# Performance work log

Measured on AMD Instinct MI355X. Metric: run time of the kernel, lower is better.

## Reference

```python
import jax, jax.numpy as jnp
import numpy as np

D_IN = 1024
D_OUT = 1024
N = 4096


def setup_inputs() -> dict:
    key = jax.random.key(0)
    kx, kq, kk, kv = jax.random.split(key, 4)
    s = 1.0 / np.sqrt(D_IN)
    return {
        "x": jax.random.normal(kx, (N, D_IN), dtype=jnp.float32),
        # nn.Linear weights stored as [d_out, d_in]
        "wq": jax.random.uniform(kq, (D_OUT, D_IN), dtype=jnp.float32, minval=-s, maxval=s),
        "wk": jax.random.uniform(kk, (D_OUT, D_IN), dtype=jnp.float32, minval=-s, maxval=s),
        "wv": jax.random.uniform(kv, (D_OUT, D_IN), dtype=jnp.float32, minval=-s, maxval=s),
    }


def reference(x, wq, wk, wv):
    q = x @ wq.T  # [N, d_out]
    k = x @ wk.T
    v = x @ wv.T
    scores = q @ k.T  # [N, N]
    weights = jax.nn.softmax(scores / jnp.sqrt(jnp.asarray(k.shape[-1], x.dtype)), axis=-1)
    return weights @ v  # [N, d_out]
```

## Files before the change

### kernel.cpp

```cpp
#include <hip/hip_runtime.h>
#include <cstdint>

#define NTOK 4096
#define DMODEL 1024

typedef __bf16 bf16x8 __attribute__((ext_vector_type(8)));
typedef float f32x4 __attribute__((ext_vector_type(4)));

__device__ __forceinline__ unsigned short f32_to_bf16(float f) {
    unsigned int u = __float_as_uint(f);
    unsigned int r = 0x7FFFu + ((u >> 16) & 1u);
    return (unsigned short)((u + r) >> 16);
}

__global__ __launch_bounds__(256) void cvt_f32_bf16(const float* __restrict__ in,
                                                    unsigned short* __restrict__ out,
                                                    int n4) {
    int i = blockIdx.x * 256 + threadIdx.x;
    if (i >= n4) return;
    float4 v = reinterpret_cast<const float4*>(in)[i];
    ushort4 o;
    o.x = f32_to_bf16(v.x);
    o.y = f32_to_bf16(v.y);
    o.z = f32_to_bf16(v.z);
    o.w = f32_to_bf16(v.w);
    reinterpret_cast<ushort4*>(out)[i] = o;
}

#define BM 128
#define BN 128
#define BK 64

#define STAGE_TILES(Ablk, lda, Bblk, ldb, k0)                                        \
    _Pragma("unroll") for (int i = 0; i < 4; ++i) {                                  \
        const int c = tid + i * 256;                                                 \
        const int row = c >> 3;                                                      \
        const int jl = (c & 7) ^ (row & 7);                                          \
        const unsigned short* ga = (Ablk) + (size_t)row * (lda) + ((k0) + jl * 8);   \
        const unsigned short* gb = (Bblk) + (size_t)row * (ldb) + ((k0) + jl * 8);   \
        __builtin_amdgcn_global_load_lds(                                            \
            (const __attribute__((address_space(1))) void*)ga,                       \
            (__attribute__((address_space(3))) void*)(&As[c * 8]), 16, 0, 0);        \
        __builtin_amdgcn_global_load_lds(                                            \
            (const __attribute__((address_space(1))) void*)gb,                       \
            (__attribute__((address_space(3))) void*)(&Bs[c * 8]), 16, 0, 0);        \
    }

#define COMPUTE_TILE()                                                               \
    _Pragma("unroll") for (int ks = 0; ks < 2; ++ks) {                               \
        bf16x8 af[4], bfr[4];                                                        \
        _Pragma("unroll") for (int m = 0; m < 4; ++m) {                              \
            const int row = wr * 64 + m * 16 + (lane & 15);                          \
            const int ch = (ks * 4 + (lane >> 4)) ^ (row & 7);                       \
            af[m] = *reinterpret_cast<const bf16x8*>(                                \
                reinterpret_cast<const char*>(As) + row * 128 + ch * 16);            \
        }                                                                            \
        _Pragma("unroll") for (int n = 0; n < 4; ++n) {                              \
            const int row = wc * 64 + n * 16 + (lane & 15);                          \
            const int ch = (ks * 4 + (lane >> 4)) ^ (row & 7);                       \
            bfr[n] = *reinterpret_cast<const bf16x8*>(                               \
                reinterpret_cast<const char*>(Bs) + row * 128 + ch * 16);            \
        }                                                                            \
        _Pragma("unroll") for (int m = 0; m < 4; ++m)                                \
            _Pragma("unroll") for (int n = 0; n < 4; ++n)                            \
                acc[m][n] = __builtin_amdgcn_mfma_f32_16x16x32_bf16(                 \
                    af[m], bfr[n], acc[m][n], 0, 0, 0);                              \
    }

__global__ __launch_bounds__(256, 2) void gemm_scores(
    const unsigned short* __restrict__ QK, float* __restrict__ S) {
    __shared__ __align__(16) unsigned short As[BM * BK];
    __shared__ __align__(16) unsigned short Bs[BN * BK];
    const int tid = threadIdx.x;
    const int lane = tid & 63;
    const int wave = tid >> 6;
    const int wr = wave >> 1, wc = wave & 1;

    const int id = blockIdx.x;
    const int g = id & 7, s = id >> 3;
    const int bx = s >> 2;
    const int by = (g << 2) + (s & 3);

    const unsigned short* Ablk = QK + (size_t)by * BM * 2048;
    const unsigned short* Bblk = QK + 1024 + (size_t)bx * BN * 2048;
    f32x4 acc[4][4] = {};

    for (int k0 = 0; k0 < DMODEL; k0 += BK) {
        STAGE_TILES(Ablk, 2048, Bblk, 2048, k0)
        __syncthreads();
        COMPUTE_TILE()
        __syncthreads();
    }

    const int col0 = bx * BN + wc * 64 + (lane & 15);
    const int row0 = by * BM + wr * 64 + ((lane >> 4) << 2);
#pragma unroll
    for (int m = 0; m < 4; ++m)
#pragma unroll
        for (int n = 0; n < 4; ++n)
#pragma unroll
            for (int r = 0; r < 4; ++r)
                S[(size_t)(row0 + m * 16 + r) * NTOK + (col0 + n * 16)] = acc[m][n][r];
}

__global__ __launch_bounds__(256, 2) void gemm_qkv(
    const unsigned short* __restrict__ xb, const unsigned short* __restrict__ Wb,
    unsigned short* __restrict__ QK, unsigned short* __restrict__ Vt) {
    __shared__ __align__(16) unsigned short As[BM * BK];
    __shared__ __align__(16) unsigned short Bs[BN * BK];
    const int tid = threadIdx.x;
    const int lane = tid & 63;
    const int wave = tid >> 6;
    const int wr = wave >> 1, wc = wave & 1;

    const int id = blockIdx.x;
    const int g = id & 7, s = id >> 3;
    const int bx = s % 24;
    const int by = (g << 2) + s / 24;

    const unsigned short* Ablk = xb + (size_t)by * BM * DMODEL;
    const unsigned short* Bblk = Wb + (size_t)bx * BN * DMODEL;
    f32x4 acc[4][4] = {};

    for (int k0 = 0; k0 < DMODEL; k0 += BK) {
        STAGE_TILES(Ablk, DMODEL, Bblk, DMODEL, k0)
        __syncthreads();
        COMPUTE_TILE()
        __syncthreads();
    }

    const int colw = wc * 64 + (lane & 15);
    const int row0 = by * BM + wr * 64 + ((lane >> 4) << 2);
    if (bx < 16) {
        const int col0 = bx * 128 + colw;
#pragma unroll
        for (int m = 0; m < 4; ++m)
#pragma unroll
            for (int n = 0; n < 4; ++n)
#pragma unroll
                for (int r = 0; r < 4; ++r)
                    QK[(size_t)(row0 + m * 16 + r) * 2048 + (col0 + n * 16)] =
                        f32_to_bf16(acc[m][n][r]);
    } else {
        const int vrow0 = (bx - 16) * 128 + colw;
#pragma unroll
        for (int m = 0; m < 4; ++m)
#pragma unroll
            for (int n = 0; n < 4; ++n) {
                ushort4 o;
                o.x = f32_to_bf16(acc[m][n][0]);
                o.y = f32_to_bf16(acc[m][n][1]);
                o.z = f32_to_bf16(acc[m][n][2]);
                o.w = f32_to_bf16(acc[m][n][3]);
                *reinterpret_cast<ushort4*>(
                    &Vt[(size_t)(vrow0 + n * 16) * NTOK + (row0 + m * 16)]) = o;
            }
    }
}

__global__ __launch_bounds__(256, 2) void gemm_pv(
    const unsigned short* __restrict__ P, const unsigned short* __restrict__ Vt,
    float* __restrict__ C) {
    __shared__ __align__(16) unsigned short As[BM * BK];
    __shared__ __align__(16) unsigned short Bs[BN * BK];
    const int tid = threadIdx.x;
    const int lane = tid & 63;
    const int wave = tid >> 6;
    const int wr = wave >> 1, wc = wave & 1;

    const int id = blockIdx.x;
    const int g = id & 7, s = id >> 3;
    const int bx = s & 7;
    const int by = (g << 2) + (s >> 3);

    const unsigned short* Ablk = P + (size_t)by * BM * (2 * NTOK);
    const unsigned short* Bblk = Vt + (size_t)bx * BN * NTOK;
    f32x4 acc[4][4] = {};

    for (int k0 = 0; k0 < NTOK; k0 += BK) {
        STAGE_TILES(Ablk, 2 * NTOK, Bblk, NTOK, k0)
        __syncthreads();
        COMPUTE_TILE()
        __syncthreads();
    }

    const int col0 = bx * BN + wc * 64 + (lane & 15);
    const int row0 = by * BM + wr * 64 + ((lane >> 4) << 2);
#pragma unroll
    for (int m = 0; m < 4; ++m)
#pragma unroll
        for (int n = 0; n < 4; ++n)
#pragma unroll
            for (int r = 0; r < 4; ++r)
                C[(size_t)(row0 + m * 16 + r) * DMODEL + (col0 + n * 16)] = acc[m][n][r];
}

__global__ __launch_bounds__(256) void softmax_rows(float* __restrict__ S, int N) {
    const int row = blockIdx.x;
    float* s = S + (size_t)row * N;
    const int t = threadIdx.x;

    float v[16];
    float mx = -1e30f;
#pragma unroll
    for (int i = 0; i < 4; ++i) {
        float4 x = reinterpret_cast<const float4*>(s)[t + i * 256];
        v[i * 4 + 0] = x.x;
        v[i * 4 + 1] = x.y;
        v[i * 4 + 2] = x.z;
        v[i * 4 + 3] = x.w;
        mx = fmaxf(mx, fmaxf(fmaxf(x.x, x.y), fmaxf(x.z, x.w)));
    }
#pragma unroll
    for (int off = 32; off; off >>= 1) mx = fmaxf(mx, __shfl_xor(mx, off));
    __shared__ float redm[4];
    if (!(t & 63)) redm[t >> 6] = mx;
    __syncthreads();
    mx = fmaxf(fmaxf(redm[0], redm[1]), fmaxf(redm[2], redm[3]));

    float sum = 0.f;
#pragma unroll
    for (int i = 0; i < 16; ++i) {
        v[i] = __expf((v[i] - mx) * 0.03125f);
        sum += v[i];
    }
#pragma unroll
    for (int off = 32; off; off >>= 1) sum += __shfl_xor(sum, off);
    __shared__ float reds[4];
    if (!(t & 63)) reds[t >> 6] = sum;
    __syncthreads();
    sum = (reds[0] + reds[1]) + (reds[2] + reds[3]);
    const float inv = 1.0f / sum;

    unsigned short* p = reinterpret_cast<unsigned short*>(s);
#pragma unroll
    for (int i = 0; i < 4; ++i) {
        ushort4 o;
        o.x = f32_to_bf16(v[i * 4 + 0] * inv);
        o.y = f32_to_bf16(v[i * 4 + 1] * inv);
        o.z = f32_to_bf16(v[i * 4 + 2] * inv);
        o.w = f32_to_bf16(v[i * 4 + 3] * inv);
        reinterpret_cast<ushort4*>(p)[t + i * 256] = o;
    }
}

extern "C" void kernel_launch(void* const* d_in, const int* in_sizes, int n_in,
                              void* d_out, int out_size, void* d_ws, size_t ws_size,
                              hipStream_t stream) {
    (void)in_sizes; (void)n_in; (void)out_size; (void)ws_size;
    const float* x = (const float*)d_in[0];
    const float* wq = (const float*)d_in[1];
    const float* wk = (const float*)d_in[2];
    const float* wv = (const float*)d_in[3];
    float* out = (float*)d_out;

    const size_t MB = 1ull << 20;
    char* w = (char*)d_ws;
    unsigned short* xb = (unsigned short*)(w + 0 * MB);
    unsigned short* Wb = (unsigned short*)(w + 8 * MB);
    unsigned short* QK = (unsigned short*)(w + 14 * MB);
    unsigned short* Vt = (unsigned short*)(w + 30 * MB);
    float* S           = (float*)(w + 38 * MB);

    cvt_f32_bf16<<<4096, 256, 0, stream>>>(x, xb, (NTOK * DMODEL) / 4);
    cvt_f32_bf16<<<1024, 256, 0, stream>>>(wq, Wb, (DMODEL * DMODEL) / 4);
    cvt_f32_bf16<<<1024, 256, 0, stream>>>(wk, Wb + DMODEL * DMODEL, (DMODEL * DMODEL) / 4);
    cvt_f32_bf16<<<1024, 256, 0, stream>>>(wv, Wb + 2 * DMODEL * DMODEL, (DMODEL * DMODEL) / 4);

    gemm_qkv<<<768, 256, 0, stream>>>(xb, Wb, QK, Vt);

    gemm_scores<<<1024, 256, 0, stream>>>(QK, S);

    softmax_rows<<<NTOK, 256, 0, stream>>>(S, NTOK);

    gemm_pv<<<256, 256, 0, stream>>>((const unsigned short*)S, Vt, out);
}
```

Baseline: 229.1 us.

## Double-buffer LDS tiles in all GEMMs and halve PV tile width for more blocks

Adds ping-pong LDS buffers to the QKV, scores and PV GEMMs so global-to-LDS loads for the next K tile are issued while MFMAs run on the current one, removing one barrier per step. The PV GEMM also shrinks its N tile from 128 to 64 and launches 512 blocks instead of 256, so the machine is filled better for that long-K GEMM. This doubles LDS use per block and can limit occupancy, and the smaller PV tile reloads P more often.

```diff
diff --git a/kernel.cpp b/kernel.cpp
--- a/kernel.cpp
+++ b/kernel.cpp
@@ -31,7 +31,7 @@
 #define BN 128
 #define BK 64
 
-#define STAGE_TILES(Ablk, lda, Bblk, ldb, k0)                                        \
+#define STAGE_DB(As_, Bs_, Ablk, lda, Bblk, ldb, k0)                                 \
     _Pragma("unroll") for (int i = 0; i < 4; ++i) {                                  \
         const int c = tid + i * 256;                                                 \
         const int row = c >> 3;                                                      \
@@ -40,26 +40,26 @@
         const unsigned short* gb = (Bblk) + (size_t)row * (ldb) + ((k0) + jl * 8);   \
         __builtin_amdgcn_global_load_lds(                                            \
             (const __attribute__((address_space(1))) void*)ga,                       \
-            (__attribute__((address_space(3))) void*)(&As[c * 8]), 16, 0, 0);        \
+            (__attribute__((address_space(3))) void*)(&(As_)[c * 8]), 16, 0, 0);     \
         __builtin_amdgcn_global_load_lds(                                            \
             (const __attribute__((address_space(1))) void*)gb,                       \
-            (__attribute__((address_space(3))) void*)(&Bs[c * 8]), 16, 0, 0);        \
-    }
-
-#define COMPUTE_TILE()                                                               \
+            (__attribute__((address_space(3))) void*)(&(Bs_)[c * 8]), 16, 0, 0);     \
+    }
+
+#define COMPUTE_DB(As_, Bs_)                                                         \
     _Pragma("unroll") for (int ks = 0; ks < 2; ++ks) {                               \
         bf16x8 af[4], bfr[4];                                                        \
         _Pragma("unroll") for (int m = 0; m < 4; ++m) {                              \
             const int row = wr * 64 + m * 16 + (lane & 15);                          \
             const int ch = (ks * 4 + (lane >> 4)) ^ (row & 7);                       \
             af[m] = *reinterpret_cast<const bf16x8*>(                                \
-                reinterpret_cast<const char*>(As) + row * 128 + ch * 16);            \
+                reinterpret_cast<const char*>(As_) + row * 128 + ch * 16);           \
         }                                                                            \
         _Pragma("unroll") for (int n = 0; n < 4; ++n) {                              \
             const int row = wc * 64 + n * 16 + (lane & 15);                          \
             const int ch = (ks * 4 + (lane >> 4)) ^ (row & 7);                       \
             bfr[n] = *reinterpret_cast<const bf16x8*>(                               \
-                reinterpret_cast<const char*>(Bs) + row * 128 + ch * 16);            \
+                reinterpret_cast<const char*>(Bs_) + row * 128 + ch * 16);           \
         }                                                                            \
         _Pragma("unroll") for (int m = 0; m < 4; ++m)                                \
             _Pragma("unroll") for (int n = 0; n < 4; ++n)                            \
@@ -69,8 +69,8 @@
 
 __global__ __launch_bounds__(256, 2) void gemm_scores(
     const unsigned short* __restrict__ QK, float* __restrict__ S) {
-    __shared__ __align__(16) unsigned short As[BM * BK];
-    __shared__ __align__(16) unsigned short Bs[BN * BK];
+    __shared__ __align__(16) unsigned short As0[BM * BK], Bs0[BN * BK];
+    __shared__ __align__(16) unsigned short As1[BM * BK], Bs1[BN * BK];
     const int tid = threadIdx.x;
     const int lane = tid & 63;
     const int wave = tid >> 6;
@@ -85,10 +85,15 @@
     const unsigned short* Bblk = QK + 1024 + (size_t)bx * BN * 2048;
     f32x4 acc[4][4] = {};
 
-    for (int k0 = 0; k0 < DMODEL; k0 += BK) {
-        STAGE_TILES(Ablk, 2048, Bblk, 2048, k0)
-        __syncthreads();
-        COMPUTE_TILE()
+    STAGE_DB(As0, Bs0, Ablk, 2048, Bblk, 2048, 0)
+    __syncthreads();
+#pragma unroll 1
+    for (int t = 0; t < 16; t += 2) {
+        STAGE_DB(As1, Bs1, Ablk, 2048, Bblk, 2048, (t + 1) * BK)
+        COMPUTE_DB(As0, Bs0)
+        __syncthreads();
+        if (t + 2 < 16) STAGE_DB(As0, Bs0, Ablk, 2048, Bblk, 2048, (t + 2) * BK)
+        COMPUTE_DB(As1, Bs1)
         __syncthreads();
     }
 
@@ -106,8 +111,8 @@
 __global__ __launch_bounds__(256, 2) void gemm_qkv(
     const unsigned short* __restrict__ xb, const unsigned short* __restrict__ Wb,
     unsigned short* __restrict__ QK, unsigned short* __restrict__ Vt) {
-    __shared__ __align__(16) unsigned short As[BM * BK];
-    __shared__ __align__(16) unsigned short Bs[BN * BK];
+    __shared__ __align__(16) unsigned short As0[BM * BK], Bs0[BN * BK];
+    __shared__ __align__(16) unsigned short As1[BM * BK], Bs1[BN * BK];
     const int tid = threadIdx.x;
     const int lane = tid & 63;
     const int wave = tid >> 6;
@@ -122,10 +127,15 @@
     const unsigned short* Bblk = Wb + (size_t)bx * BN * DMODEL;
     f32x4 acc[4][4] = {};
 
-    for (int k0 = 0; k0 < DMODEL; k0 += BK) {
-        STAGE_TILES(Ablk, DMODEL, Bblk, DMODEL, k0)
-        __syncthreads();
-        COMPUTE_TILE()
+    STAGE_DB(As0, Bs0, Ablk, DMODEL, Bblk, DMODEL, 0)
+    __syncthreads();
+#pragma unroll 1
+    for (int t = 0; t < 16; t += 2) {
+        STAGE_DB(As1, Bs1, Ablk, DMODEL, Bblk, DMODEL, (t + 1) * BK)
+        COMPUTE_DB(As0, Bs0)
+        __syncthreads();
+        if (t + 2 < 16) STAGE_DB(As0, Bs0, Ablk, DMODEL, Bblk, DMODEL, (t + 2) * BK)
+        COMPUTE_DB(As1, Bs1)
         __syncthreads();
     }
 
@@ -158,11 +168,52 @@
     }
 }
 
+#define PV_STAGE(As_, Bs_, k0)                                                        \
+    _Pragma("unroll") for (int i = 0; i < 4; ++i) {                                   \
+        const int c = tid + i * 256;                                                  \
+        const int row = c >> 3;                                                       \
+        const int jl = (c & 7) ^ (row & 7);                                           \
+        const unsigned short* ga = Ablk + (size_t)row * (2 * NTOK) + ((k0) + jl * 8); \
+        __builtin_amdgcn_global_load_lds(                                             \
+            (const __attribute__((address_space(1))) void*)ga,                        \
+            (__attribute__((address_space(3))) void*)(&(As_)[c * 8]), 16, 0, 0);      \
+    }                                                                                 \
+    _Pragma("unroll") for (int i = 0; i < 2; ++i) {                                   \
+        const int c = tid + i * 256;                                                  \
+        const int row = c >> 3;                                                       \
+        const int jl = (c & 7) ^ (row & 7);                                           \
+        const unsigned short* gb = Bblk + (size_t)row * NTOK + ((k0) + jl * 8);       \
+        __builtin_amdgcn_global_load_lds(                                             \
+            (const __attribute__((address_space(1))) void*)gb,                        \
+            (__attribute__((address_space(3))) void*)(&(Bs_)[c * 8]), 16, 0, 0);      \
+    }
+
+#define PV_COMPUTE(As_, Bs_)                                                          \
+    _Pragma("unroll") for (int ks = 0; ks < 2; ++ks) {                                \
+        bf16x8 af[4], bfr[2];                                                         \
+        _Pragma("unroll") for (int m = 0; m < 4; ++m) {                               \
+            const int row = wr * 64 + m * 16 + (lane & 15);                           \
+            const int ch = (ks * 4 + (lane >> 4)) ^ (row & 7);                        \
+            af[m] = *reinterpret_cast<const bf16x8*>(                                 \
+                reinterpret_cast<const char*>(As_) + row * 128 + ch * 16);            \
+        }                                                                             \
+        _Pragma("unroll") for (int n = 0; n < 2; ++n) {                               \
+            const int row = wc * 32 + n * 16 + (lane & 15);                           \
+            const int ch = (ks * 4 + (lane >> 4)) ^ (row & 7);                        \
+            bfr[n] = *reinterpret_cast<const bf16x8*>(                                \
+                reinterpret_cast<const char*>(Bs_) + row * 128 + ch * 16);            \
+        }                                                                             \
+        _Pragma("unroll") for (int m = 0; m < 4; ++m)                                 \
+            _Pragma("unroll") for (int n = 0; n < 2; ++n)                             \
+                acc[m][n] = __builtin_amdgcn_mfma_f32_16x16x32_bf16(                  \
+                    af[m], bfr[n], acc[m][n], 0, 0, 0);                               \
+    }
+
 __global__ __launch_bounds__(256, 2) void gemm_pv(
     const unsigned short* __restrict__ P, const unsigned short* __restrict__ Vt,
     float* __restrict__ C) {
-    __shared__ __align__(16) unsigned short As[BM * BK];
-    __shared__ __align__(16) unsigned short Bs[BN * BK];
+    __shared__ __align__(16) unsigned short As0[128 * BK], Bs0[64 * BK];
+    __shared__ __align__(16) unsigned short As1[128 * BK], Bs1[64 * BK];
     const int tid = threadIdx.x;
     const int lane = tid & 63;
     const int wave = tid >> 6;
@@ -170,26 +221,31 @@
 
     const int id = blockIdx.x;
     const int g = id & 7, s = id >> 3;
-    const int bx = s & 7;
-    const int by = (g << 2) + (s >> 3);
-
-    const unsigned short* Ablk = P + (size_t)by * BM * (2 * NTOK);
-    const unsigned short* Bblk = Vt + (size_t)bx * BN * NTOK;
-    f32x4 acc[4][4] = {};
-
-    for (int k0 = 0; k0 < NTOK; k0 += BK) {
-        STAGE_TILES(Ablk, 2 * NTOK, Bblk, NTOK, k0)
-        __syncthreads();
-        COMPUTE_TILE()
-        __syncthreads();
-    }
-
-    const int col0 = bx * BN + wc * 64 + (lane & 15);
-    const int row0 = by * BM + wr * 64 + ((lane >> 4) << 2);
+    const int bx = s & 15;
+    const int by = (g << 2) + (s >> 4);
+
+    const unsigned short* Ablk = P + (size_t)by * 128 * (2 * NTOK);
+    const unsigned short* Bblk = Vt + (size_t)bx * 64 * NTOK;
+    f32x4 acc[4][2] = {};
+
+    PV_STAGE(As0, Bs0, 0)
+    __syncthreads();
+#pragma unroll 1
+    for (int t = 0; t < 64; t += 2) {
+        PV_STAGE(As1, Bs1, (t + 1) * BK)
+        PV_COMPUTE(As0, Bs0)
+        __syncthreads();
+        if (t + 2 < 64) PV_STAGE(As0, Bs0, (t + 2) * BK)
+        PV_COMPUTE(As1, Bs1)
+        __syncthreads();
+    }
+
+    const int col0 = bx * 64 + wc * 32 + (lane & 15);
+    const int row0 = by * 128 + wr * 64 + ((lane >> 4) << 2);
 #pragma unroll
     for (int m = 0; m < 4; ++m)
 #pragma unroll
-        for (int n = 0; n < 4; ++n)
+        for (int n = 0; n < 2; ++n)
 #pragma unroll
             for (int r = 0; r < 4; ++r)
                 C[(size_t)(row0 + m * 16 + r) * DMODEL + (col0 + n * 16)] = acc[m][n][r];
@@ -273,5 +329,5 @@
 
     softmax_rows<<<NTOK, 256, 0, stream>>>(S, NTOK);
 
-    gemm_pv<<<256, 256, 0, stream>>>((const unsigned short*)S, Vt, out);
-}
+    gemm_pv<<<512, 256, 0, stream>>>((const unsigned short*)S, Vt, out);
+}
```

Result: faster. 220.7 us (-3.7%).
